# Kernel optimization log

Measured on AMD Instinct MI355X. Metric: run time of the kernel, lower is better.

## Reference

```python
import jax, jax.numpy as jnp
import numpy as np

B, S, E, H, D = 4, 2048, 2048, 16, 128
EPS = 1e-6


def _rope_cache(seq_len, dim, base=10000.0):
    # standard rotary cache, half-split layout matching rotate_half
    inv_freq = 1.0 / (base ** (np.arange(0, dim // 2, dtype=np.float32) / (dim // 2)))
    t = np.arange(seq_len, dtype=np.float32)
    freqs = np.outer(t, inv_freq)                     # [S, D/2]
    emb = np.concatenate([freqs, freqs], axis=-1)     # [S, D]
    cos = jnp.asarray(np.cos(emb))[None, :, None, :]  # [1, S, 1, D]
    sin = jnp.asarray(np.sin(emb))[None, :, None, :]
    return cos, sin


def setup_inputs() -> dict:
    key = jax.random.key(0)
    ks = jax.random.split(key, 5)
    scale = 1.0 / np.sqrt(E)
    x = jax.random.normal(ks[0], (B, S, E), dtype=jnp.float32)
    Wq = jax.random.normal(ks[1], (E, E), dtype=jnp.float32) * scale
    Wk = jax.random.normal(ks[2], (E, E), dtype=jnp.float32) * scale
    Wv = jax.random.normal(ks[3], (E, E), dtype=jnp.float32) * scale
    Wo = jax.random.normal(ks[4], (E, E), dtype=jnp.float32) * scale
    cos, sin = _rope_cache(S, D)
    return {"x": x, "cos": cos, "sin": sin, "Wq": Wq, "Wk": Wk, "Wv": Wv, "Wo": Wo}


def _rotate_half(t):
    d = t.shape[-1] // 2
    return jnp.concatenate([-t[..., d:], t[..., :d]], axis=-1)


def _rms_norm(t, eps):
    return t * jax.lax.rsqrt(jnp.mean(t * t, axis=-1, keepdims=True) + eps)


def reference(x, cos, sin, Wq, Wk, Wv, Wo):
    b, s, _ = x.shape
    # QKV projections (Linear without bias: x @ W.T), reshape to heads
    q = (x @ Wq.T).reshape(b, s, H, D)
    k = (x @ Wk.T).reshape(b, s, H, D)
    v = (x @ Wv.T).reshape(b, s, H, D)
    # RoPE then QK RMSNorm (no learned scale)
    q = _rms_norm(q * cos + _rotate_half(q) * sin, EPS)
    k = _rms_norm(k * cos + _rotate_half(k) * sin, EPS)
    # non-causal SDPA
    scores = jnp.einsum("bqhd,bkhd->bhqk", q, k) / np.sqrt(D)
    probs = jax.nn.softmax(scores, axis=-1)
    y = jnp.einsum("bhqk,bkhd->bqhd", probs, v).reshape(b, s, H * D)
    return y @ Wo.T
```

## Files before the change

### kernel.cpp

```cpp
#include <hip/hip_runtime.h>
#include <hip/hip_bf16.h>
#include <math.h>


typedef __bf16 bf16_t;
typedef __bf16 bf16x2 __attribute__((ext_vector_type(2)));
typedef __bf16 bf16x4 __attribute__((ext_vector_type(4)));
typedef __bf16 bf16x8 __attribute__((ext_vector_type(8)));
typedef float f32x2 __attribute__((ext_vector_type(2)));
typedef float f32x4 __attribute__((ext_vector_type(4)));
typedef float f32x16 __attribute__((ext_vector_type(16)));
typedef unsigned int u32;
typedef u32 u32x4 __attribute__((ext_vector_type(4)));

typedef __attribute__((address_space(1))) const void gas_cvoid;
typedef __attribute__((address_space(3))) void las_void;

#define MFMA16(a, b, c) __builtin_amdgcn_mfma_f32_16x16x32_bf16((a), (b), (c), 0, 0, 0)
#define MFMA32(a, b, c) __builtin_amdgcn_mfma_f32_32x32x16_bf16((a), (b), (c), 0, 0, 0)

__device__ __forceinline__ void gload16(const void* g, void* l) {
  __builtin_amdgcn_global_load_lds((gas_cvoid*)g, (las_void*)l, 16, 0, 0);
}

__global__ __launch_bounds__(256) void cvt_bf16(const float* __restrict__ in,
                                                bf16_t* __restrict__ out) {
  const size_t i = ((size_t)blockIdx.x * 256 + threadIdx.x) * 4;
  f32x4 v = *(const f32x4*)&in[i];
  bf16x4 o;
#pragma unroll
  for (int j = 0; j < 4; ++j) o[j] = (bf16_t)v[j];
  *(bf16x4*)&out[i] = o;
}

template <int MODE, typename CT, int NT_T>
__global__ __launch_bounds__(256, 2) void gemm_bt(const bf16_t* __restrict__ A,
                                                  const bf16_t* __restrict__ Bt,
                                                  CT* __restrict__ C) {
  constexpr int K = 2048;
  __shared__ __attribute__((aligned(16))) bf16_t lds_a[128 * 32];
  __shared__ __attribute__((aligned(16))) bf16_t lds_b[128 * 32];
  const int tid = threadIdx.x;
  const int wave = tid >> 6, lane = tid & 63;
  const int bid = blockIdx.x;
  const int swz = (bid & 7) * 128 + (bid >> 3);
  const int m0 = (swz / NT_T) * 128, n0 = (swz % NT_T) * 128;

  const bf16_t* aS = A + (size_t)(m0 + (tid >> 2)) * K + (tid & 3) * 8;
  const bf16_t* bS = Bt + (size_t)(n0 + (tid >> 2)) * K + (tid & 3) * 8;
  char* la = (char*)lds_a + wave * 1024;
  char* lb = (char*)lds_b + wave * 1024;

  const int wm = wave >> 1, wn = wave & 1;
  const int l15 = lane & 15, l4 = lane >> 4;
  const int rA = (wm * 64 + l15) * 32 + l4 * 8;
  const int rB = (wn * 64 + l15) * 32 + l4 * 8;

  f32x4 acc[4][4] = {};

  for (int kt = 0; kt < K / 32; ++kt) {
    gload16(aS, la);
    gload16(aS + (size_t)64 * K, la + 4096);
    gload16(bS, lb);
    gload16(bS + (size_t)64 * K, lb + 4096);
    aS += 32;
    bS += 32;
    __syncthreads();
    bf16x8 af[4], bfr[4];
#pragma unroll
    for (int mi = 0; mi < 4; ++mi) af[mi] = *(const bf16x8*)&lds_a[rA + mi * 16 * 32];
#pragma unroll
    for (int ni = 0; ni < 4; ++ni) bfr[ni] = *(const bf16x8*)&lds_b[rB + ni * 16 * 32];
#pragma unroll
    for (int mi = 0; mi < 4; ++mi)
#pragma unroll
      for (int ni = 0; ni < 4; ++ni) acc[mi][ni] = MFMA16(af[mi], bfr[ni], acc[mi][ni]);
    __syncthreads();
  }

  const int rBase = m0 + wm * 64 + l4 * 4;
  const int cBase = n0 + wn * 64 + l15;
#pragma unroll
  for (int mi = 0; mi < 4; ++mi)
#pragma unroll
    for (int ni = 0; ni < 4; ++ni)
#pragma unroll
      for (int j = 0; j < 4; ++j) {
        const int r = rBase + mi * 16 + j;
        const int c = cBase + ni * 16;
        const CT v = (CT)acc[mi][ni][j];
        if (MODE == 0) {
          const int b = r >> 11, s = r & 2047, hh = c >> 7, d = c & 127;
          C[(((size_t)(b * 16 + hh)) * 2048 + s) * 128 + d] = v;
        } else if (MODE == 1) {
          C[(size_t)r * 2048 + c] = v;
        } else {
          const int hh = r >> 7, dd = r & 127, b = c >> 11, s = c & 2047;
          C[((size_t)(b * 16 + hh) * 128 + dd) * 2048 + s] = v;
        }
      }
}

__global__ __launch_bounds__(256) void rope_rms(bf16_t* __restrict__ T,
                                                const float* __restrict__ Cs,
                                                const float* __restrict__ Sn) {
  const int wave = threadIdx.x >> 6, lane = threadIdx.x & 63;
#pragma unroll 1
  for (int rr = 0; rr < 8; ++rr) {
    const size_t row = (size_t)blockIdx.x * 32 + wave * 8 + rr;
    const int s = (int)(row & 2047);
    bf16_t* p = &T[row * 128 + 2 * lane];
    const float a0 = (float)p[0], a1 = (float)p[1];
    f32x2 cv = *(const f32x2*)&Cs[(size_t)s * 128 + 2 * lane];
    f32x2 sv = *(const f32x2*)&Sn[(size_t)s * 128 + 2 * lane];
    const float p0 = __shfl_xor(a0, 32);
    const float p1 = __shfl_xor(a1, 32);
    const float sg = (lane < 32) ? -1.f : 1.f;
    const float r0 = a0 * cv.x + sg * p0 * sv.x;
    const float r1 = a1 * cv.y + sg * p1 * sv.y;
    float ss = r0 * r0 + r1 * r1;
#pragma unroll
    for (int off = 1; off < 64; off <<= 1) ss += __shfl_xor(ss, off);
    const float inv = rsqrtf(ss * (1.0f / 128.0f) + 1e-6f);
    p[0] = (bf16_t)(r0 * inv);
    p[1] = (bf16_t)(r1 * inv);
  }
}

__global__ __launch_bounds__(512, 2) void attn_fwd(const bf16_t* __restrict__ Q,
                                                   const bf16_t* __restrict__ K,
                                                   const bf16_t* __restrict__ Vt,
                                                   bf16_t* __restrict__ Y) {
  __shared__ __attribute__((aligned(16))) bf16_t ldsK[2][64 * 128];
  __shared__ __attribute__((aligned(16))) bf16_t ldsV[2][128 * 64];
  const int tid = threadIdx.x, wave = tid >> 6, lane = tid & 63;
  const int l31 = lane & 31, hi = lane >> 5;
  const int pid = blockIdx.x;
  const int bh = (pid & 7) * 8 + ((pid >> 3) & 7);
  const int qb = pid >> 6;
  const int b = bh >> 4, h = bh & 15;
  const bf16_t* Qh = Q + (size_t)bh * 2048 * 128;
  const bf16_t* Kh = K + (size_t)bh * 2048 * 128;
  const bf16_t* Vh = Vt + (size_t)bh * 128 * 2048;
  const int q0 = qb * 256 + wave * 32;

  bf16x8 qf[8];
#pragma unroll
  for (int dk = 0; dk < 8; ++dk)
    qf[dk] = *(const bf16x8*)&Qh[(size_t)(q0 + l31) * 128 + dk * 16 + hi * 8];

  f32x16 ot[4] = {};
  float m_r = -1e30f, l_r = 0.f;
  const float scale = 0.08838834764831845f;

  auto stage = [&](int kt, int bu) {
#pragma unroll
    for (int i = 0; i < 2; ++i) {
      const int G = wave * 64 + lane + i * 512;
      char* dstK = (char*)&ldsK[bu][0] + (wave * 64 + i * 512) * 16;
      char* dstV = (char*)&ldsV[bu][0] + (wave * 64 + i * 512) * 16;
      const int kvr = G >> 4, glk = G & 15;
      gload16(Kh + (size_t)(kt * 64 + kvr) * 128 + ((glk ^ (kvr & 7)) * 8), dstK);
      const int dr = G >> 3, glv = G & 7;
      gload16(Vh + (size_t)dr * 2048 + kt * 64 + ((glv ^ (dr & 7)) * 8), dstV);
    }
  };

  stage(0, 0);
  __syncthreads();

  for (int kt = 0; kt < 32; ++kt) {
    const int bu = kt & 1;
    if (kt < 31) stage(kt + 1, bu ^ 1);

    f32x16 sa0 = {}, sa1 = {};
    const int r7 = l31 & 7;
#pragma unroll
    for (int dk = 0; dk < 8; ++dk) {
      const int g = ((dk << 1) | hi) ^ r7;
      bf16x8 kf0 = *(const bf16x8*)&ldsK[bu][l31 * 128 + g * 8];
      bf16x8 kf1 = *(const bf16x8*)&ldsK[bu][(32 + l31) * 128 + g * 8];
      sa0 = MFMA32(kf0, qf[dk], sa0);
      sa1 = MFMA32(kf1, qf[dk], sa1);
    }

    float mx = sa0[0];
#pragma unroll
    for (int j = 1; j < 16; ++j) mx = fmaxf(mx, sa0[j]);
#pragma unroll
    for (int j = 0; j < 16; ++j) mx = fmaxf(mx, sa1[j]);
    mx = fmaxf(mx, __shfl_xor(mx, 32));
    mx *= scale;
    if (__any(mx > m_r + 8.f)) {
      const float mn = fmaxf(m_r, mx);
      const float corr = __expf(m_r - mn);
      m_r = mn;
      l_r *= corr;
#pragma unroll
      for (int db = 0; db < 4; ++db)
#pragma unroll
        for (int j = 0; j < 16; ++j) ot[db][j] *= corr;
    }
    u32 w[2][8];
    float ssum = 0.f;
#pragma unroll
    for (int i = 0; i < 8; ++i) {
      const float p0 = __expf(sa0[2 * i] * scale - m_r);
      const float p1 = __expf(sa0[2 * i + 1] * scale - m_r);
      const float p2 = __expf(sa1[2 * i] * scale - m_r);
      const float p3 = __expf(sa1[2 * i + 1] * scale - m_r);
      ssum += (p0 + p1) + (p2 + p3);
      bf16x2 t0, t1;
      t0[0] = (bf16_t)p0; t0[1] = (bf16_t)p1;
      t1[0] = (bf16_t)p2; t1[1] = (bf16_t)p3;
      w[0][i] = __builtin_bit_cast(u32, t0);
      w[1][i] = __builtin_bit_cast(u32, t1);
    }
    ssum += __shfl_xor(ssum, 32);
    l_r += ssum;

#pragma unroll
    for (int ks = 0; ks < 4; ++ks) {
      const int t = ks >> 1, k4 = (ks & 1) * 4;
      const u32 x0 = (u32)__shfl_xor((int)w[t][k4 + 0], 32);
      const u32 x1 = (u32)__shfl_xor((int)w[t][k4 + 1], 32);
      const u32 x2 = (u32)__shfl_xor((int)w[t][k4 + 2], 32);
      const u32 x3 = (u32)__shfl_xor((int)w[t][k4 + 3], 32);
      u32x4 fw;
      fw.x = hi ? x2 : w[t][k4 + 0];
      fw.y = hi ? x3 : w[t][k4 + 1];
      fw.z = hi ? w[t][k4 + 2] : x0;
      fw.w = hi ? w[t][k4 + 3] : x1;
      const bf16x8 pf = __builtin_bit_cast(bf16x8, fw);
      const int gv = ((ks << 1) | hi) ^ r7;
#pragma unroll
      for (int db = 0; db < 4; ++db) {
        bf16x8 vf = *(const bf16x8*)&ldsV[bu][(db * 32 + l31) * 64 + gv * 8];
        ot[db] = MFMA32(vf, pf, ot[db]);
      }
    }
    __syncthreads();
  }

  const float rl = 1.f / l_r;
  const size_t yrow = ((size_t)(b * 2048 + q0 + l31) * 16 + h) * 128;
#pragma unroll
  for (int db = 0; db < 4; ++db)
#pragma unroll
    for (int g2 = 0; g2 < 4; ++g2) {
      bf16x4 ov;
#pragma unroll
      for (int j = 0; j < 4; ++j) ov[j] = (bf16_t)(ot[db][g2 * 4 + j] * rl);
      *(bf16x4*)&Y[yrow + db * 32 + g2 * 8 + hi * 4] = ov;
    }
}

extern "C" void kernel_launch(void* const* d_in, const int* in_sizes, int n_in,
                              void* d_out, int out_size, void* d_ws, size_t ws_size,
                              hipStream_t stream) {
  const float* x = (const float*)d_in[0];
  const float* cs = (const float*)d_in[1];
  const float* sn = (const float*)d_in[2];
  const float* Wq = (const float*)d_in[3];
  const float* Wk = (const float*)d_in[4];
  const float* Wv = (const float*)d_in[5];
  const float* Wo = (const float*)d_in[6];

  bf16_t* ws = (bf16_t*)d_ws;
  const size_t TSZ = (size_t)4 * 2048 * 2048;
  const size_t WSZ = (size_t)2048 * 2048;
  bf16_t* xb = ws;
  bf16_t* Wqb = ws + TSZ;
  bf16_t* Wkb = Wqb + WSZ;
  bf16_t* Wvb = Wkb + WSZ;
  bf16_t* Wob = Wvb + WSZ;
  bf16_t* Qb = ws + 2 * TSZ;
  bf16_t* Kb = Qb + TSZ;
  bf16_t* Vtb = Kb + TSZ;
  bf16_t* Yb = xb;

  cvt_bf16<<<16384, 256, 0, stream>>>(x, xb);
  cvt_bf16<<<4096, 256, 0, stream>>>(Wq, Wqb);
  cvt_bf16<<<4096, 256, 0, stream>>>(Wk, Wkb);
  cvt_bf16<<<4096, 256, 0, stream>>>(Wv, Wvb);
  cvt_bf16<<<4096, 256, 0, stream>>>(Wo, Wob);

  gemm_bt<0, bf16_t, 16><<<1024, 256, 0, stream>>>(xb, Wqb, Qb);
  gemm_bt<0, bf16_t, 16><<<1024, 256, 0, stream>>>(xb, Wkb, Kb);
  gemm_bt<2, bf16_t, 64><<<1024, 256, 0, stream>>>(Wvb, xb, Vtb);
  rope_rms<<<4096, 256, 0, stream>>>(Qb, cs, sn);
  rope_rms<<<4096, 256, 0, stream>>>(Kb, cs, sn);
  attn_fwd<<<512, 512, 0, stream>>>(Qb, Kb, Vtb, Yb);
  gemm_bt<1, float, 16><<<1024, 256, 0, stream>>>(Yb, Wob, (float*)d_out);
}
```

Baseline: 571.5 us.

## Use 256x256 double-buffered GEMM tiles, permlane swaps, setprio, and fused weight conversion

Replaces the 128x128 single-buffered GEMM with a 512-thread, 256x256-tile kernel. It uses double-buffered 128KB LDS with XOR swizzling, BK=64, staged prefetch interleaved with MFMA phases, and s_setprio around the MFMAs. In attention, the cross-half shuffles become v_permlane32_swap, the row max uses a tree reduction, and setprio wraps the MFMA blocks. The four weight conversions merge into one launch. The larger tiles raise data reuse and overlap loads with compute, but give only 256 blocks and use large LDS, which limits occupancy.

```diff
diff --git a/kernel.cpp b/kernel.cpp
--- a/kernel.cpp
+++ b/kernel.cpp
@@ -22,6 +22,9 @@
 __device__ __forceinline__ void gload16(const void* g, void* l) {
   __builtin_amdgcn_global_load_lds((gas_cvoid*)g, (las_void*)l, 16, 0, 0);
 }
+__device__ __forceinline__ void pl32(u32& a, u32& b) {
+  asm volatile("v_permlane32_swap_b32 %0, %1" : "+v"(a), "+v"(b));
+}
 
 __global__ __launch_bounds__(256) void cvt_bf16(const float* __restrict__ in,
                                                 bf16_t* __restrict__ out) {
@@ -32,56 +35,114 @@
   for (int j = 0; j < 4; ++j) o[j] = (bf16_t)v[j];
   *(bf16x4*)&out[i] = o;
 }
+__global__ __launch_bounds__(256) void cvt_w4(const float* __restrict__ w0,
+                                              const float* __restrict__ w1,
+                                              const float* __restrict__ w2,
+                                              const float* __restrict__ w3,
+                                              bf16_t* __restrict__ o0,
+                                              bf16_t* __restrict__ o1,
+                                              bf16_t* __restrict__ o2,
+                                              bf16_t* __restrict__ o3) {
+  const int which = blockIdx.x >> 12;
+  const float* in = which == 0 ? w0 : which == 1 ? w1 : which == 2 ? w2 : w3;
+  bf16_t* out = which == 0 ? o0 : which == 1 ? o1 : which == 2 ? o2 : o3;
+  const size_t i = ((size_t)(blockIdx.x & 4095) * 256 + threadIdx.x) * 4;
+  f32x4 v = *(const f32x4*)&in[i];
+  bf16x4 o;
+#pragma unroll
+  for (int j = 0; j < 4; ++j) o[j] = (bf16_t)v[j];
+  *(bf16x4*)&out[i] = o;
+}
 
 template <int MODE, typename CT, int NT_T>
-__global__ __launch_bounds__(256, 2) void gemm_bt(const bf16_t* __restrict__ A,
-                                                  const bf16_t* __restrict__ Bt,
-                                                  CT* __restrict__ C) {
+__global__ __launch_bounds__(512, 2) void gemm8(const bf16_t* __restrict__ A,
+                                                const bf16_t* __restrict__ Bt,
+                                                CT* __restrict__ C) {
   constexpr int K = 2048;
-  __shared__ __attribute__((aligned(16))) bf16_t lds_a[128 * 32];
-  __shared__ __attribute__((aligned(16))) bf16_t lds_b[128 * 32];
+  __shared__ __attribute__((aligned(16))) char lds[131072];
   const int tid = threadIdx.x;
   const int wave = tid >> 6, lane = tid & 63;
   const int bid = blockIdx.x;
-  const int swz = (bid & 7) * 128 + (bid >> 3);
-  const int m0 = (swz / NT_T) * 128, n0 = (swz % NT_T) * 128;
-
-  const bf16_t* aS = A + (size_t)(m0 + (tid >> 2)) * K + (tid & 3) * 8;
-  const bf16_t* bS = Bt + (size_t)(n0 + (tid >> 2)) * K + (tid & 3) * 8;
-  char* la = (char*)lds_a + wave * 1024;
-  char* lb = (char*)lds_b + wave * 1024;
-
-  const int wm = wave >> 1, wn = wave & 1;
+  const int swz = (bid & 7) * 32 + (bid >> 3);
+  const int m0 = (swz / NT_T) * 256, n0 = (swz % NT_T) * 256;
+
+  const int srow = tid >> 3;
+  const int scol = ((tid & 7) ^ (srow & 7)) * 8;
+  const bf16_t* aBase = A + (size_t)(m0 + srow) * K + scol;
+  const bf16_t* bBase = Bt + (size_t)(n0 + srow) * K + scol;
+
+  const int wm = wave >> 2, wn = wave & 3;
   const int l15 = lane & 15, l4 = lane >> 4;
-  const int rA = (wm * 64 + l15) * 32 + l4 * 8;
-  const int rB = (wn * 64 + l15) * 32 + l4 * 8;
-
-  f32x4 acc[4][4] = {};
-
-  for (int kt = 0; kt < K / 32; ++kt) {
-    gload16(aS, la);
-    gload16(aS + (size_t)64 * K, la + 4096);
-    gload16(bS, lb);
-    gload16(bS + (size_t)64 * K, lb + 4096);
-    aS += 32;
-    bS += 32;
-    __syncthreads();
-    bf16x8 af[4], bfr[4];
-#pragma unroll
-    for (int mi = 0; mi < 4; ++mi) af[mi] = *(const bf16x8*)&lds_a[rA + mi * 16 * 32];
-#pragma unroll
-    for (int ni = 0; ni < 4; ++ni) bfr[ni] = *(const bf16x8*)&lds_b[rB + ni * 16 * 32];
-#pragma unroll
-    for (int mi = 0; mi < 4; ++mi)
-#pragma unroll
-      for (int ni = 0; ni < 4; ++ni) acc[mi][ni] = MFMA16(af[mi], bfr[ni], acc[mi][ni]);
-    __syncthreads();
+  const int axor = l15 & 7;
+
+  f32x4 acc[8][4] = {};
+
+  auto stageA = [&](int tt, int nbuf) {
+#pragma unroll
+    for (int h = 0; h < 2; ++h)
+#pragma unroll
+      for (int cc = 0; cc < 2; ++cc)
+        gload16(aBase + (size_t)(h * 128 + cc * 64) * K + tt * 64,
+                lds + nbuf * 65536 + h * 16384 + cc * 8192 + wave * 1024);
+  };
+  auto stageB = [&](int tt, int nbuf) {
+#pragma unroll
+    for (int h = 0; h < 2; ++h)
+#pragma unroll
+      for (int cc = 0; cc < 2; ++cc)
+        gload16(bBase + (size_t)(h * 128 + cc * 64) * K + tt * 64,
+                lds + nbuf * 65536 + 32768 + h * 16384 + cc * 8192 + wave * 1024);
+  };
+
+  stageA(0, 0);
+  stageB(0, 0);
+  __syncthreads();
+
+  for (int t = 0; t < 32; ++t) {
+    const int buf = t & 1, nbuf = buf ^ 1;
+    const char* la = lds + buf * 65536 + wm * 16384;
+    const char* lb = lds + buf * 65536 + 32768 + (wn >> 1) * 16384 + (wn & 1) * 8192;
+    bf16x8 bF[4][2];
+#pragma unroll
+    for (int q = 0; q < 4; ++q) {
+      bf16x8 aF[2][2];
+#pragma unroll
+      for (int dm = 0; dm < 2; ++dm)
+#pragma unroll
+        for (int kk = 0; kk < 2; ++kk)
+          aF[dm][kk] = *(const bf16x8*)(la + ((q * 2 + dm) * 16 + l15) * 128 +
+                                        ((kk * 4 + l4) ^ axor) * 16);
+      if (q == 0) {
+#pragma unroll
+        for (int ni = 0; ni < 4; ++ni)
+#pragma unroll
+          for (int kk = 0; kk < 2; ++kk)
+            bF[ni][kk] = *(const bf16x8*)(lb + (ni * 16 + l15) * 128 +
+                                          ((kk * 4 + l4) ^ axor) * 16);
+        if (t < 31) stageA(t + 1, nbuf);
+      }
+      if (q == 1 && t < 31) stageB(t + 1, nbuf);
+      __builtin_amdgcn_s_barrier();
+      __builtin_amdgcn_s_setprio(1);
+#pragma unroll
+      for (int kk = 0; kk < 2; ++kk)
+#pragma unroll
+        for (int dm = 0; dm < 2; ++dm)
+#pragma unroll
+          for (int ni = 0; ni < 4; ++ni)
+            acc[q * 2 + dm][ni] = MFMA16(aF[dm][kk], bF[ni][kk], acc[q * 2 + dm][ni]);
+      __builtin_amdgcn_s_setprio(0);
+      if (q < 3)
+        __builtin_amdgcn_s_barrier();
+      else
+        __syncthreads();
+    }
   }
 
-  const int rBase = m0 + wm * 64 + l4 * 4;
+  const int rBase = m0 + wm * 128 + l4 * 4;
   const int cBase = n0 + wn * 64 + l15;
 #pragma unroll
-  for (int mi = 0; mi < 4; ++mi)
+  for (int mi = 0; mi < 8; ++mi)
 #pragma unroll
     for (int ni = 0; ni < 4; ++ni)
 #pragma unroll
@@ -175,6 +236,7 @@
 
     f32x16 sa0 = {}, sa1 = {};
     const int r7 = l31 & 7;
+    __builtin_amdgcn_s_setprio(1);
 #pragma unroll
     for (int dk = 0; dk < 8; ++dk) {
       const int g = ((dk << 1) | hi) ^ r7;
@@ -183,14 +245,16 @@
       sa0 = MFMA32(kf0, qf[dk], sa0);
       sa1 = MFMA32(kf1, qf[dk], sa1);
     }
-
-    float mx = sa0[0];
-#pragma unroll
-    for (int j = 1; j < 16; ++j) mx = fmaxf(mx, sa0[j]);
-#pragma unroll
-    for (int j = 0; j < 16; ++j) mx = fmaxf(mx, sa1[j]);
-    mx = fmaxf(mx, __shfl_xor(mx, 32));
-    mx *= scale;
+    __builtin_amdgcn_s_setprio(0);
+
+    float tm[16];
+#pragma unroll
+    for (int j = 0; j < 16; ++j) tm[j] = fmaxf(sa0[j], sa1[j]);
+#pragma unroll
+    for (int s = 8; s; s >>= 1)
+#pragma unroll
+      for (int j = 0; j < s; ++j) tm[j] = fmaxf(tm[j], tm[j + s]);
+    float mx = fmaxf(tm[0], __shfl_xor(tm[0], 32)) * scale;
     if (__any(mx > m_r + 8.f)) {
       const float mn = fmaxf(m_r, mx);
       const float corr = __expf(m_r - mn);
@@ -221,23 +285,22 @@
 
 #pragma unroll
     for (int ks = 0; ks < 4; ++ks) {
-      const int t = ks >> 1, k4 = (ks & 1) * 4;
-      const u32 x0 = (u32)__shfl_xor((int)w[t][k4 + 0], 32);
-      const u32 x1 = (u32)__shfl_xor((int)w[t][k4 + 1], 32);
-      const u32 x2 = (u32)__shfl_xor((int)w[t][k4 + 2], 32);
-      const u32 x3 = (u32)__shfl_xor((int)w[t][k4 + 3], 32);
+      const int tsel = ks >> 1, k4 = (ks & 1) * 4;
+      u32 a0 = w[tsel][k4 + 0], b0 = w[tsel][k4 + 2];
+      u32 a1 = w[tsel][k4 + 1], b1 = w[tsel][k4 + 3];
+      pl32(a0, b0);
+      pl32(a1, b1);
       u32x4 fw;
-      fw.x = hi ? x2 : w[t][k4 + 0];
-      fw.y = hi ? x3 : w[t][k4 + 1];
-      fw.z = hi ? w[t][k4 + 2] : x0;
-      fw.w = hi ? w[t][k4 + 3] : x1;
+      fw.x = a0; fw.y = a1; fw.z = b0; fw.w = b1;
       const bf16x8 pf = __builtin_bit_cast(bf16x8, fw);
       const int gv = ((ks << 1) | hi) ^ r7;
+      __builtin_amdgcn_s_setprio(1);
 #pragma unroll
       for (int db = 0; db < 4; ++db) {
         bf16x8 vf = *(const bf16x8*)&ldsV[bu][(db * 32 + l31) * 64 + gv * 8];
         ot[db] = MFMA32(vf, pf, ot[db]);
       }
+      __builtin_amdgcn_s_setprio(0);
     }
     __syncthreads();
   }
@@ -280,16 +343,13 @@
   bf16_t* Yb = xb;
 
   cvt_bf16<<<16384, 256, 0, stream>>>(x, xb);
-  cvt_bf16<<<4096, 256, 0, stream>>>(Wq, Wqb);
-  cvt_bf16<<<4096, 256, 0, stream>>>(Wk, Wkb);
-  cvt_bf16<<<4096, 256, 0, stream>>>(Wv, Wvb);
-  cvt_bf16<<<4096, 256, 0, stream>>>(Wo, Wob);
-
-  gemm_bt<0, bf16_t, 16><<<1024, 256, 0, stream>>>(xb, Wqb, Qb);
-  gemm_bt<0, bf16_t, 16><<<1024, 256, 0, stream>>>(xb, Wkb, Kb);
-  gemm_bt<2, bf16_t, 64><<<1024, 256, 0, stream>>>(Wvb, xb, Vtb);
+  cvt_w4<<<16384, 256, 0, stream>>>(Wq, Wk, Wv, Wo, Wqb, Wkb, Wvb, Wob);
+
+  gemm8<0, bf16_t, 8><<<256, 512, 0, stream>>>(xb, Wqb, Qb);
+  gemm8<0, bf16_t, 8><<<256, 512, 0, stream>>>(xb, Wkb, Kb);
+  gemm8<2, bf16_t, 32><<<256, 512, 0, stream>>>(Wvb, xb, Vtb);
   rope_rms<<<4096, 256, 0, stream>>>(Qb, cs, sn);
   rope_rms<<<4096, 256, 0, stream>>>(Kb, cs, sn);
   attn_fwd<<<512, 512, 0, stream>>>(Qb, Kb, Vtb, Yb);
-  gemm_bt<1, float, 16><<<1024, 256, 0, stream>>>(Yb, Wob, (float*)d_out);
-}
+  gemm8<1, float, 8><<<256, 512, 0, stream>>>(Yb, Wob, (float*)d_out);
+}
```

Measured after the change: 489.6 us. 1.17x faster.
